# Kernel optimization log

Measured on AMD Instinct MI355X. Metric: run time of the kernel, lower is better.

The kernel has to match this reference:

```python
import jax, jax.numpy as jnp
import numpy as np

GAMMA = 0.99
EPS = 1e-07


def setup_inputs() -> dict:
    key = jax.random.key(0)
    k1, k2, k3 = jax.random.split(key, 3)
    V, D = 8192, 256
    b, s = 8, 16
    x = jax.random.normal(k1, (b, D, s, s, s), dtype=jnp.float32)
    weight = jax.random.normal(k2, (V, D), dtype=jnp.float32)
    N = jnp.zeros((V,), dtype=jnp.float32)
    z_avg = jax.random.normal(k3, (V, D), dtype=jnp.float32)
    return {"x": x, "weight": weight, "N": N, "z_avg": z_avg}


def reference(x, weight, N, z_avg):
    V, D = weight.shape
    b, c, x1, x2, x3 = x.shape
    # (b, c, x1, x2, x3) -> (b*x1*x2*x3, D), channels last
    flat = jnp.transpose(x, (0, 2, 3, 4, 1)).reshape(-1, D)
    # pairwise squared L2 distances: ||z||^2 - 2 z.W^T + ||W||^2
    dists = (
        jnp.sum(flat * flat, axis=1, keepdims=True)
        - 2.0 * (flat @ weight.T)
        + jnp.sum(weight * weight, axis=1)[None, :]
    )
    idx = jnp.argmin(dists, axis=1)  # same tie-break (first) as torch.max(-d)
    quant = weight[idx].reshape(b, x1, x2, x3, D)
    quant = jnp.transpose(quant, (0, 4, 1, 2, 3))  # back to (b, c, x1, x2, x3)

    # EMA cluster statistics (training-mode update) via scatter-reduce,
    # equivalent to the torch one-hot matmuls encode_onehot.sum(0) and
    # flat_inputs.T @ encode_onehot.
    counts = jax.ops.segment_sum(jnp.ones(flat.shape[0], dtype=flat.dtype), idx, num_segments=V)
    enc_sum = jax.ops.segment_sum(flat, idx, num_segments=V)  # (V, D)
    new_N = GAMMA * N + (1.0 - GAMMA) * counts
    new_z_avg = GAMMA * z_avg + (1.0 - GAMMA) * enc_sum
    n = jnp.sum(new_N)
    w = (new_N + EPS) / (n + V * EPS) * n
    new_weight = new_z_avg / w[:, None]

    quant_st = jax.lax.stop_gradient(quant - x) + x  # straight-through
    quant_diff = jnp.mean(jnp.square(x - jax.lax.stop_gradient(quant)))
    enc_idx = idx.reshape(b, x1, x2, x3)
    return quant_st, enc_idx, quant_diff, new_N, new_z_avg, new_weight
```

## Files before the change

### kernel.cpp

```cpp
#include <hip/hip_runtime.h>

#define V_CODES 8192
#define D_DIM   256
#define SPATIAL 4096
#define M_ROWS  32768
#define NELEM   8388608

static constexpr float GAMMA_F = 0.99f;
static constexpr float OMG_F   = (float)(1.0 - 0.99);
static constexpr float EPS_F   = 1e-7f;
static constexpr float VEPS_F  = (float)(8192 * 1e-7);

static constexpr size_t OFF_QUANT = 0;
static constexpr size_t OFF_IDX   = 8388608;
static constexpr size_t OFF_QDIFF = 8421376;
static constexpr size_t OFF_NN    = 8421377;
static constexpr size_t OFF_ZAVG  = 8429569;
static constexpr size_t OFF_W     = 10526721;

typedef _Float16 f16x8 __attribute__((ext_vector_type(8)));
typedef float    f32x4 __attribute__((ext_vector_type(4)));

#define GLL(gp, lp) __builtin_amdgcn_global_load_lds( \
    (const __attribute__((address_space(1))) unsigned int*)(gp), \
    (__attribute__((address_space(3))) unsigned int*)(lp), 16, 0, 0)

__global__ void k_wnorm(const float* __restrict__ W, float* __restrict__ wnorm) {
    int v = blockIdx.x * 4 + (threadIdx.x >> 6);
    int lane = threadIdx.x & 63;
    float4 w4 = *(const float4*)(W + (size_t)v * D_DIM + lane * 4);
    float s = w4.x * w4.x + w4.y * w4.y + w4.z * w4.z + w4.w * w4.w;
    #pragma unroll
    for (int m = 32; m > 0; m >>= 1) s += __shfl_xor(s, m, 64);
    if (lane == 0) wnorm[v] = s;
}

__global__ void k_split_w(const float* __restrict__ W, _Float16* __restrict__ Wh,
                          _Float16* __restrict__ Wl) {
    size_t i8 = ((size_t)blockIdx.x * 256 + threadIdx.x) * 8;
    float4 a = *(const float4*)(W + i8);
    float4 b = *(const float4*)(W + i8 + 4);
    float v[8] = {a.x, a.y, a.z, a.w, b.x, b.y, b.z, b.w};
    f16x8 hi, lo;
    #pragma unroll
    for (int j = 0; j < 8; j++) {
        _Float16 h = (_Float16)v[j];
        hi[j] = h;
        lo[j] = (_Float16)(v[j] - (float)h);
    }
    *(f16x8*)(Wh + i8) = hi;
    *(f16x8*)(Wl + i8) = lo;
}

__global__ void k_split_x(const float* __restrict__ X, _Float16* __restrict__ Xh,
                          _Float16* __restrict__ Xl) {
    int bid  = blockIdx.x;
    int lane = threadIdx.x & 63;
    int kg   = (bid & 1) * 4 + (threadIdx.x >> 6);
    int m    = (bid >> 1) * 64 + lane;
    int b  = m >> 12;
    int sp = m & 4095;
    const float* src = X + (size_t)b * (D_DIM * SPATIAL) + (size_t)(kg * 32) * SPATIAL + sp;
    float v[32];
    #pragma unroll
    for (int j = 0; j < 32; j++) v[j] = src[(size_t)j * SPATIAL];
    _Float16* dh = Xh + (size_t)m * D_DIM + kg * 32;
    _Float16* dl = Xl + (size_t)m * D_DIM + kg * 32;
    #pragma unroll
    for (int c = 0; c < 4; c++) {
        f16x8 hi, lo;
        #pragma unroll
        for (int j = 0; j < 8; j++) {
            float x = v[c * 8 + j];
            _Float16 h = (_Float16)x;
            hi[j] = h;
            lo[j] = (_Float16)(x - (float)h);
        }
        *(f16x8*)(dh + c * 8) = hi;
        *(f16x8*)(dl + c * 8) = lo;
    }
}

__device__ inline unsigned long long packkey(float s, int v) {
    unsigned u = __float_as_uint(s);
    u = (u & 0x80000000u) ? ~u : (u | 0x80000000u);
    return ((unsigned long long)u << 32) | (unsigned)v;
}

__global__ __launch_bounds__(256, 2) void k_mfma_argmin(
        const _Float16* __restrict__ Xh, const _Float16* __restrict__ Xl,
        const _Float16* __restrict__ Wh, const _Float16* __restrict__ Wl,
        const float* __restrict__ wnorm, unsigned long long* __restrict__ best) {
    __shared__ __align__(16) _Float16 lds[16384];
    const int tid  = threadIdx.x;
    const int wid  = tid >> 6;
    const int lane = tid & 63;
    const int wy = wid >> 1, wx = wid & 1;
    const int lrow = lane & 15, lq = lane >> 4;
    const int m0 = blockIdx.y * 128;
    const int v0 = blockIdx.x * 128;

    f32x4 acc[4][4] = {};

    const _Float16* planes[4] = {Xh, Xl, Wh, Wl};
    const _Float16* P = planes[wid];
    const int rowb = (wid < 2 ? m0 : v0) + lrow;

    for (int k0 = 0; k0 < D_DIM; k0 += 32) {
        __syncthreads();
        #pragma unroll
        for (int sub = 0; sub < 8; sub++) {
            const _Float16* g = P + (size_t)(rowb + sub * 16) * D_DIM + k0 + lq * 8;
            GLL(g, &lds[(wid * 8 + sub) * 512]);
        }
        __syncthreads();
        f16x8 ah[4], al[4], bh[4], bl[4];
        #pragma unroll
        for (int i = 0; i < 4; i++) {
            ah[i] = *(const f16x8*)&lds[(      wy * 4 + i) * 512 + lane * 8];
            al[i] = *(const f16x8*)&lds[( 8 + wy * 4 + i) * 512 + lane * 8];
            bh[i] = *(const f16x8*)&lds[(16 + wx * 4 + i) * 512 + lane * 8];
            bl[i] = *(const f16x8*)&lds[(24 + wx * 4 + i) * 512 + lane * 8];
        }
        #pragma unroll
        for (int mi = 0; mi < 4; mi++)
            #pragma unroll
            for (int vi = 0; vi < 4; vi++) {
                acc[mi][vi] = __builtin_amdgcn_mfma_f32_16x16x32_f16(ah[mi], bh[vi], acc[mi][vi], 0, 0, 0);
                acc[mi][vi] = __builtin_amdgcn_mfma_f32_16x16x32_f16(al[mi], bh[vi], acc[mi][vi], 0, 0, 0);
                acc[mi][vi] = __builtin_amdgcn_mfma_f32_16x16x32_f16(ah[mi], bl[vi], acc[mi][vi], 0, 0, 0);
            }
    }

    float wnv[4];
    #pragma unroll
    for (int vi = 0; vi < 4; vi++) wnv[vi] = wnorm[v0 + (wx * 4 + vi) * 16 + lrow];

    #pragma unroll
    for (int mi = 0; mi < 4; mi++) {
        #pragma unroll
        for (int r = 0; r < 4; r++) {
            unsigned long long k = ~0ull;
            #pragma unroll
            for (int vi = 0; vi < 4; vi++) {
                int v = v0 + (wx * 4 + vi) * 16 + lrow;
                float s = wnv[vi] - 2.0f * acc[mi][vi][r];
                unsigned long long key = packkey(s, v);
                k = key < k ? key : k;
            }
            #pragma unroll
            for (int msk = 1; msk < 16; msk <<= 1) {
                unsigned long long o = __shfl_xor(k, msk, 64);
                k = o < k ? o : k;
            }
            if (lrow == 0) {
                int m = m0 + (wy * 4 + mi) * 16 + lq * 4 + r;
                atomicMin(&best[m], k);
            }
        }
    }
}

__global__ void k_count(const unsigned long long* __restrict__ best,
                        int* __restrict__ counts, float* __restrict__ out) {
    int m = blockIdx.x * 256 + threadIdx.x;
    int v = (int)(unsigned)(best[m] & 0xFFFFFFFFull);
    atomicAdd(&counts[v], 1);
    out[OFF_IDX + m] = (float)v;
}

__global__ void k_prefix(const int* __restrict__ counts, int* __restrict__ offsets,
                         int* __restrict__ cursor) {
    __shared__ int tsum[256];
    int t = threadIdx.x;
    int local[32];
    int s = 0;
    #pragma unroll
    for (int i = 0; i < 32; i++) { local[i] = s; s += counts[t * 32 + i]; }
    tsum[t] = s;
    __syncthreads();
    if (t == 0) {
        int run = 0;
        for (int i = 0; i < 256; i++) { int c = tsum[i]; tsum[i] = run; run += c; }
    }
    __syncthreads();
    int base = tsum[t];
    #pragma unroll
    for (int i = 0; i < 32; i++) {
        int o = base + local[i];
        offsets[t * 32 + i] = o;
        cursor[t * 32 + i]  = o;
    }
}

__global__ void k_fill(const unsigned long long* __restrict__ best,
                       int* __restrict__ cursor, int* __restrict__ bin) {
    int m = blockIdx.x * 256 + threadIdx.x;
    int v = (int)(unsigned)(best[m] & 0xFFFFFFFFull);
    int pos = atomicAdd(&cursor[v], 1);
    bin[pos] = m;
}

__global__ void k_codes(const _Float16* __restrict__ Xh, const _Float16* __restrict__ Xl,
                        const float* __restrict__ N, const float* __restrict__ zavg,
                        const int* __restrict__ counts, const int* __restrict__ offsets,
                        const int* __restrict__ bin, float* __restrict__ out) {
    int v = blockIdx.x;
    int d = threadIdx.x;
    int cnt = counts[v];
    int off = offsets[v];
    float s = 0.0f;
    for (int r = 0; r < cnt; r++) {
        int m = bin[off + r];
        s += (float)Xh[(size_t)m * D_DIM + d] + (float)Xl[(size_t)m * D_DIM + d];
    }
    out[OFF_ZAVG + (size_t)v * D_DIM + d] = GAMMA_F * zavg[(size_t)v * D_DIM + d] + OMG_F * s;
    if (d == 0) out[OFF_NN + v] = GAMMA_F * N[v] + OMG_F * (float)cnt;
}

__global__ void k_quant(const float* __restrict__ X, const float* __restrict__ W,
                        const unsigned long long* __restrict__ best, float* __restrict__ out,
                        float* __restrict__ ws_scal) {
    int e4 = blockIdx.x * 256 + threadIdx.x;
    int e  = e4 * 4;
    int sp = e & 4095;
    int bd = e >> 12;
    int d  = bd & 255;
    int b  = bd >> 8;
    int mb = b * SPATIAL + sp;
    float4 x4 = *(const float4*)(X + e);
    float q[4];
    float p = 0.0f;
    #pragma unroll
    for (int j = 0; j < 4; j++) {
        int v = (int)(unsigned)(best[mb + j] & 0xFFFFFFFFull);
        float wv = W[(size_t)v * D_DIM + d];
        float xv = (j == 0) ? x4.x : (j == 1) ? x4.y : (j == 2) ? x4.z : x4.w;
        q[j] = (wv - xv) + xv;
        float df = xv - wv;
        p = fmaf(df, df, p);
    }
    *(float4*)(out + OFF_QUANT + e) = make_float4(q[0], q[1], q[2], q[3]);
    #pragma unroll
    for (int msk = 32; msk > 0; msk >>= 1) p += __shfl_xor(p, msk, 64);
    __shared__ float red[4];
    int lane = threadIdx.x & 63, w = threadIdx.x >> 6;
    if (lane == 0) red[w] = p;
    __syncthreads();
    if (threadIdx.x == 0)
        atomicAdd(ws_scal, red[0] + red[1] + red[2] + red[3]);
}

__global__ void k_finalize_n(const float* __restrict__ outNN, float* __restrict__ ws_scal,
                             float* __restrict__ out_qdiff) {
    __shared__ float red[256];
    float s = 0.0f;
    for (int v = threadIdx.x; v < V_CODES; v += 256) s += outNN[v];
    red[threadIdx.x] = s;
    __syncthreads();
    #pragma unroll
    for (int t = 128; t > 0; t >>= 1) {
        if (threadIdx.x < t) red[threadIdx.x] += red[threadIdx.x + t];
        __syncthreads();
    }
    if (threadIdx.x == 0) {
        ws_scal[1] = red[0];
        out_qdiff[0] = ws_scal[0] * (1.0f / 8388608.0f);
    }
}

__global__ void k_weight(const float* __restrict__ zavg_out, const float* __restrict__ nn_out,
                         const float* __restrict__ ws_scal, float* __restrict__ out_w) {
    int i = blockIdx.x * 256 + threadIdx.x;
    int v = i >> 8;
    float n = ws_scal[1];
    float w = (nn_out[v] + EPS_F) / (n + VEPS_F) * n;
    out_w[i] = zavg_out[i] / w;
}

extern "C" void kernel_launch(void* const* d_in, const int* in_sizes, int n_in,
                              void* d_out, int out_size, void* d_ws, size_t ws_size,
                              hipStream_t stream) {
    const float* x    = (const float*)d_in[0];
    const float* w    = (const float*)d_in[1];
    const float* N    = (const float*)d_in[2];
    const float* zavg = (const float*)d_in[3];
    float* out = (float*)d_out;
    char*  wsb = (char*)d_ws;

    float* ws_scal   = (float*)wsb;
    int*   ws_counts = (int*)(wsb + 64);
    float* ws_wnorm  = (float*)(wsb + 32832);
    int*   ws_off    = (int*)(wsb + 65600);
    int*   ws_cur    = (int*)(wsb + 98368);
    int*   ws_bin    = (int*)(wsb + 131136);
    unsigned long long* ws_best = (unsigned long long*)(wsb + 262208);
    _Float16* Xh = (_Float16*)(wsb + 524352);
    _Float16* Xl = (_Float16*)(wsb + 524352 + 16777216);
    _Float16* Wh = (_Float16*)(wsb + 524352 + 2 * 16777216);
    _Float16* Wl = (_Float16*)(wsb + 524352 + 2 * 16777216 + 4194304);

    hipMemsetAsync(wsb, 0, 32832, stream);
    hipMemsetAsync(ws_best, 0xFF, (size_t)M_ROWS * 8, stream);

    k_wnorm  <<<V_CODES / 4, 256, 0, stream>>>(w, ws_wnorm);
    k_split_w<<<(V_CODES * D_DIM) / (256 * 8), 256, 0, stream>>>(w, Wh, Wl);
    k_split_x<<<1024, 256, 0, stream>>>(x, Xh, Xl);

    dim3 grid(V_CODES / 128, M_ROWS / 128);
    k_mfma_argmin<<<grid, 256, 0, stream>>>(Xh, Xl, Wh, Wl, ws_wnorm, ws_best);

    k_count  <<<M_ROWS / 256, 256, 0, stream>>>(ws_best, ws_counts, out);
    k_prefix <<<1, 256, 0, stream>>>(ws_counts, ws_off, ws_cur);
    k_fill   <<<M_ROWS / 256, 256, 0, stream>>>(ws_best, ws_cur, ws_bin);
    k_codes  <<<V_CODES, 256, 0, stream>>>(Xh, Xl, N, zavg, ws_counts, ws_off, ws_bin, out);
    k_quant  <<<NELEM / (256 * 4), 256, 0, stream>>>(x, w, ws_best, out, ws_scal);

    k_finalize_n<<<1, 256, 0, stream>>>(out + OFF_NN, ws_scal, out + OFF_QDIFF);
    k_weight <<<(V_CODES * D_DIM) / 256, 256, 0, stream>>>(out + OFF_ZAVG, out + OFF_NN, ws_scal, out + OFF_W);
}
```

Measured before the change: 962.0 us.

## Fuse wnorm into W split, raise argmin occupancy, filter redundant atomics

The codebook norm is now computed inside the fp16 split kernel with a 32-lane shuffle reduction, which drops one launch and one extra pass over W. The MFMA argmin kernel asks for 4 blocks per CU instead of 2 and loads the B fragments one column at a time, which lowers register pressure. Before each atomicMin it reads the current best and skips the atomic when it cannot win, cutting atomic traffic. The higher occupancy target may force register spills, since 64 accumulator floats stay live per thread.

```diff
diff --git a/kernel.cpp b/kernel.cpp
--- a/kernel.cpp
+++ b/kernel.cpp
@@ -25,31 +25,27 @@
     (const __attribute__((address_space(1))) unsigned int*)(gp), \
     (__attribute__((address_space(3))) unsigned int*)(lp), 16, 0, 0)
 
-__global__ void k_wnorm(const float* __restrict__ W, float* __restrict__ wnorm) {
-    int v = blockIdx.x * 4 + (threadIdx.x >> 6);
-    int lane = threadIdx.x & 63;
-    float4 w4 = *(const float4*)(W + (size_t)v * D_DIM + lane * 4);
-    float s = w4.x * w4.x + w4.y * w4.y + w4.z * w4.z + w4.w * w4.w;
-    #pragma unroll
-    for (int m = 32; m > 0; m >>= 1) s += __shfl_xor(s, m, 64);
-    if (lane == 0) wnorm[v] = s;
-}
-
 __global__ void k_split_w(const float* __restrict__ W, _Float16* __restrict__ Wh,
-                          _Float16* __restrict__ Wl) {
-    size_t i8 = ((size_t)blockIdx.x * 256 + threadIdx.x) * 8;
+                          _Float16* __restrict__ Wl, float* __restrict__ wnorm) {
+    int t = blockIdx.x * 256 + threadIdx.x;
+    size_t i8 = (size_t)t * 8;
     float4 a = *(const float4*)(W + i8);
     float4 b = *(const float4*)(W + i8 + 4);
     float v[8] = {a.x, a.y, a.z, a.w, b.x, b.y, b.z, b.w};
     f16x8 hi, lo;
+    float s = 0.0f;
     #pragma unroll
     for (int j = 0; j < 8; j++) {
         _Float16 h = (_Float16)v[j];
         hi[j] = h;
         lo[j] = (_Float16)(v[j] - (float)h);
+        s = fmaf(v[j], v[j], s);
     }
     *(f16x8*)(Wh + i8) = hi;
     *(f16x8*)(Wl + i8) = lo;
+    #pragma unroll
+    for (int msk = 1; msk < 32; msk <<= 1) s += __shfl_xor(s, msk, 64);
+    if ((threadIdx.x & 31) == 0) wnorm[t >> 5] = s;
 }
 
 __global__ void k_split_x(const float* __restrict__ X, _Float16* __restrict__ Xh,
@@ -87,7 +83,7 @@
     return ((unsigned long long)u << 32) | (unsigned)v;
 }
 
-__global__ __launch_bounds__(256, 2) void k_mfma_argmin(
+__global__ __launch_bounds__(256, 4) void k_mfma_argmin(
         const _Float16* __restrict__ Xh, const _Float16* __restrict__ Xl,
         const _Float16* __restrict__ Wh, const _Float16* __restrict__ Wl,
         const float* __restrict__ wnorm, unsigned long long* __restrict__ best) {
@@ -114,22 +110,23 @@
             GLL(g, &lds[(wid * 8 + sub) * 512]);
         }
         __syncthreads();
-        f16x8 ah[4], al[4], bh[4], bl[4];
+        f16x8 ah[4], al[4];
         #pragma unroll
         for (int i = 0; i < 4; i++) {
-            ah[i] = *(const f16x8*)&lds[(      wy * 4 + i) * 512 + lane * 8];
-            al[i] = *(const f16x8*)&lds[( 8 + wy * 4 + i) * 512 + lane * 8];
-            bh[i] = *(const f16x8*)&lds[(16 + wx * 4 + i) * 512 + lane * 8];
-            bl[i] = *(const f16x8*)&lds[(24 + wx * 4 + i) * 512 + lane * 8];
-        }
-        #pragma unroll
-        for (int mi = 0; mi < 4; mi++)
+            ah[i] = *(const f16x8*)&lds[(     wy * 4 + i) * 512 + lane * 8];
+            al[i] = *(const f16x8*)&lds[(8 +  wy * 4 + i) * 512 + lane * 8];
+        }
+        #pragma unroll
+        for (int vi = 0; vi < 4; vi++) {
+            f16x8 bh = *(const f16x8*)&lds[(16 + wx * 4 + vi) * 512 + lane * 8];
+            f16x8 bl = *(const f16x8*)&lds[(24 + wx * 4 + vi) * 512 + lane * 8];
             #pragma unroll
-            for (int vi = 0; vi < 4; vi++) {
-                acc[mi][vi] = __builtin_amdgcn_mfma_f32_16x16x32_f16(ah[mi], bh[vi], acc[mi][vi], 0, 0, 0);
-                acc[mi][vi] = __builtin_amdgcn_mfma_f32_16x16x32_f16(al[mi], bh[vi], acc[mi][vi], 0, 0, 0);
-                acc[mi][vi] = __builtin_amdgcn_mfma_f32_16x16x32_f16(ah[mi], bl[vi], acc[mi][vi], 0, 0, 0);
+            for (int mi = 0; mi < 4; mi++) {
+                acc[mi][vi] = __builtin_amdgcn_mfma_f32_16x16x32_f16(ah[mi], bh, acc[mi][vi], 0, 0, 0);
+                acc[mi][vi] = __builtin_amdgcn_mfma_f32_16x16x32_f16(al[mi], bh, acc[mi][vi], 0, 0, 0);
+                acc[mi][vi] = __builtin_amdgcn_mfma_f32_16x16x32_f16(ah[mi], bl, acc[mi][vi], 0, 0, 0);
             }
+        }
     }
 
     float wnv[4];
@@ -155,7 +152,7 @@
             }
             if (lrow == 0) {
                 int m = m0 + (wy * 4 + mi) * 16 + lq * 4 + r;
-                atomicMin(&best[m], k);
+                if (k < best[m]) atomicMin(&best[m], k);
             }
         }
     }
@@ -303,8 +300,7 @@
     hipMemsetAsync(wsb, 0, 32832, stream);
     hipMemsetAsync(ws_best, 0xFF, (size_t)M_ROWS * 8, stream);
 
-    k_wnorm  <<<V_CODES / 4, 256, 0, stream>>>(w, ws_wnorm);
-    k_split_w<<<(V_CODES * D_DIM) / (256 * 8), 256, 0, stream>>>(w, Wh, Wl);
+    k_split_w<<<(V_CODES * D_DIM) / (256 * 8), 256, 0, stream>>>(w, Wh, Wl, ws_wnorm);
     k_split_x<<<1024, 256, 0, stream>>>(x, Xh, Xl);
 
     dim3 grid(V_CODES / 128, M_ROWS / 128);
```

Result: slower. 2.516 ms (+161.5%).
